# Kernel optimization log

Hardware: AMD Instinct MI355X
Metric: run time of the kernel (lower is better)

## Reference

```python
import jax, jax.numpy as jnp
import numpy as np

H = 64        # hidden_dim
A = 21        # N_ACTIONS
B = 262144    # batch size


def setup_inputs() -> dict:
    key = jax.random.key(0)
    ks = jax.random.split(key, 32)

    def w(k, shape):
        fan_in = shape[0]
        return (jax.random.normal(k, shape, jnp.float32) / np.float32(np.sqrt(fan_in)))

    inp = {
        "x": jax.random.normal(ks[0], (B, 2, 2), jnp.float32),
        "b_act1": jax.random.randint(ks[1], (B,), 0, A),
        "b_act2": jax.random.randint(ks[2], (B,), 0, A),
        # enc: Linear(2,H), ReLU, Linear(H,H), ReLU
        "enc_w1": w(ks[3], (2, H)), "enc_b1": jnp.zeros((H,), jnp.float32),
        "enc_w2": w(ks[4], (H, H)), "enc_b2": jnp.zeros((H,), jnp.float32),
        # q_net: Linear(H,H), ReLU, Linear(H,A)
        "q_w1": w(ks[5], (H, H)), "q_b1": jnp.zeros((H,), jnp.float32),
        "q_w2": w(ks[6], (H, A)), "q_b2": jnp.zeros((A,), jnp.float32),
        # v_net: Linear(H,H), ReLU, Linear(H,1)
        "v_w1": w(ks[7], (H, H)), "v_b1": jnp.zeros((H,), jnp.float32),
        "v_w2": w(ks[8], (H, 1)), "v_b2": jnp.zeros((1,), jnp.float32),
        # lin2: Linear(H+A,H), ReLU, Linear(H,H), ReLU, Linear(H,H)
        "l2_w1": w(ks[9], (H + A, H)), "l2_b1": jnp.zeros((H,), jnp.float32),
        "l2_w2": w(ks[10], (H, H)), "l2_b2": jnp.zeros((H,), jnp.float32),
        "l2_w3": w(ks[11], (H, H)), "l2_b3": jnp.zeros((H,), jnp.float32),
        # lin3, lin4
        "l3_w": w(ks[12], (H, H)), "l3_b": jnp.zeros((H,), jnp.float32),
        "l4_w": w(ks[13], (H, A)), "l4_b": jnp.zeros((A,), jnp.float32),
        # q_prime_net: Linear(H,2H) ELU Linear(2H,H) ELU Linear(H,H) ELU Linear(H,1)
        "qp_w1": w(ks[14], (H, 2 * H)), "qp_b1": jnp.zeros((2 * H,), jnp.float32),
        "qp_w2": w(ks[15], (2 * H, H)), "qp_b2": jnp.zeros((H,), jnp.float32),
        "qp_w3": w(ks[16], (H, H)), "qp_b3": jnp.zeros((H,), jnp.float32),
        "qp_w4": w(ks[17], (H, 1)), "qp_b4": jnp.zeros((1,), jnp.float32),
    }
    return inp


def reference(x, b_act1, b_act2,
              enc_w1, enc_b1, enc_w2, enc_b2,
              q_w1, q_b1, q_w2, q_b2,
              v_w1, v_b1, v_w2, v_b2,
              l2_w1, l2_b1, l2_w2, l2_b2, l2_w3, l2_b3,
              l3_w, l3_b, l4_w, l4_b,
              qp_w1, qp_b1, qp_w2, qp_b2, qp_w3, qp_b3, qp_w4, qp_b4):
    relu = jax.nn.relu
    elu = jax.nn.elu

    def enc(z):
        return relu(relu(z @ enc_w1 + enc_b1) @ enc_w2 + enc_b2)

    def q_net(h):
        return relu(h @ q_w1 + q_b1) @ q_w2 + q_b2

    def lin2(e):  # ends with bare Linear (no final activation)
        h = relu(e @ l2_w1 + l2_b1)
        h = relu(h @ l2_w2 + l2_b2)
        return h @ l2_w3 + l2_b3

    def q_prime(z):
        h = elu(z @ qp_w1 + qp_b1)
        h = elu(h @ qp_w2 + qp_b2)
        h = elu(h @ qp_w3 + qp_b3)
        return h @ qp_w4 + qp_b4

    h1 = enc(x[:, 0, :])  # [B,H]
    h2 = enc(x[:, 1, :])
    q1, q2 = q_net(h1), q_net(h2)              # [B,A]
    key2 = jnp.stack([h1, h2], axis=1)          # [B,2,H]
    vtot = relu((h1 + h2) @ v_w1 + v_b1) @ v_w2 + v_b2  # [B,1]

    def joint(act1, act2):
        oh1 = jax.nn.one_hot(act1, A, dtype=h1.dtype)
        oh2 = jax.nn.one_hot(act2, A, dtype=h2.dtype)
        e = jnp.stack([jnp.concatenate([h1, oh1], axis=-1),
                       jnp.concatenate([h2, oh2], axis=-1)], axis=1)  # [B,2,H+A]
        key1 = lin2(e)                              # [B,2,H]
        q = q_prime(key1.mean(axis=1))              # [B,1]
        return key1, q

    key1, joint_qs = joint(b_act1, b_act2)
    a1_max = jnp.argmax(q1, axis=1)
    a2_max = jnp.argmax(q2, axis=1)
    key1_max, joint_max_qs = joint(a1_max, a2_max)

    def q_jt(k1):
        z = key2 + k1.mean(axis=1, keepdims=True) - k1 / 2  # [B,2,H]
        return relu(z @ l3_w + l3_b) @ l4_w + l4_b           # [B,2,A]

    q_jt_alt = q_jt(key1)
    q_jt_max_alt = q_jt(key1_max)

    return (q1, q2, joint_qs, joint_max_qs, vtot, q_jt_alt, q_jt_max_alt)
```

## Files before the change

### kernel.cpp

```cpp
#include <hip/hip_runtime.h>
#include <hip/hip_bf16.h>


#define B_TOT 262144

typedef __bf16 bf16_t;
typedef __bf16 bf16x4 __attribute__((ext_vector_type(4)));
typedef __bf16 bf16x8 __attribute__((ext_vector_type(8)));
typedef float  f32x4  __attribute__((ext_vector_type(4)));

#define MFMA16(a, b, c) __builtin_amdgcn_mfma_f32_16x16x32_bf16((a), (b), (c), 0, 0, 0)

enum : int {
  OFF_VW1  = 0,
  OFF_L2W1 = 4096,
  OFF_L2W2 = 8192,
  OFF_L2W3 = 12288,
  OFF_L3W  = 16384,
  OFF_L4W  = 20480,
  OFF_QP1  = 22528,
  OFF_QP2  = 30720,
  OFF_QP3  = 38912,
  WS_ELEMS = 43008
};
#define WS_BYTES (WS_ELEMS * 2)

enum : int {
  O_Q1   = 0,
  O_Q2   = 21 * B_TOT,
  O_JQ   = 42 * B_TOT,
  O_JMQ  = 43 * B_TOT,
  O_VT   = 44 * B_TOT,
  O_QJT  = 45 * B_TOT,
  O_QJTM = 87 * B_TOT
};

struct RDesc { const float* src; int K; int N; int NT; int off; };
struct RPack { RDesc d[9]; };

__global__ void repack_kernel(RPack P, bf16_t* __restrict__ ws) {
  RDesc d = P.d[blockIdx.x];
  int n = (d.K >> 5) * d.NT * 512;
  for (int i = threadIdx.x; i < n; i += blockDim.x) {
    int j  = i & 7;
    int l  = (i >> 3) & 63;
    int t  = i >> 9;
    int nt = t % d.NT;
    int kc = t / d.NT;
    int sk = kc * 32 + 16 * (j >> 2) + 4 * (l >> 4) + (j & 3);
    int sn = nt * 16 + (l & 15);
    float v = (sn < d.N) ? d.src[sk * d.N + sn] : 0.0f;
    ws[d.off + i] = (bf16_t)v;
  }
}

struct Args {
  const float* x; const int* a1; const int* a2;
  const float* ew1; const float* eb1; const float* ew2; const float* eb2;
  const float* qw1; const float* qb1; const float* qw2; const float* qb2;
  const float* vw1; const float* vb1; const float* vw2; const float* vb2;
  const float* l2w1; const float* l2b1; const float* l2w2; const float* l2b2;
  const float* l2w3; const float* l2b3;
  const float* l3w;  const float* l3b;  const float* l4w;  const float* l4b;
  const float* qpw1; const float* qpb1; const float* qpw2; const float* qpb2;
  const float* qpw3; const float* qpb3; const float* qpw4; const float* qpb4;
  float* out; const bf16_t* ws;
};

struct __align__(16) SMem {
  bf16_t h1b[64 * 72];
  bf16_t h2b[64 * 72];
  unsigned char scr[34816];
  float  bias[768];
  bf16_t oneh[21 * 68];
  int    acts[128];
  int    amax[128];
  float  red[64][2];
  int    redi[64][2];
};

__device__ __forceinline__ float eluf(float x) { return x > 0.f ? x : expm1f(x); }

__device__ __forceinline__ void fcA64(const float* __restrict__ fin, float* __restrict__ fout,
                                      const float* __restrict__ W, const float* __restrict__ Bv,
                                      bf16_t* hb, int r, int g) {
  float2 acc[8];
#pragma unroll
  for (int i = 0; i < 8; i++) acc[i] = make_float2(Bv[g * 16 + 2 * i], Bv[g * 16 + 2 * i + 1]);
#pragma unroll 4
  for (int k4 = 0; k4 < 16; k4++) {
    float4 a = *(const float4*)(fin + r * 68 + k4 * 4);
    float av[4] = {a.x, a.y, a.z, a.w};
#pragma unroll
    for (int kk = 0; kk < 4; kk++) {
      const float2* wr = (const float2*)(W + (k4 * 4 + kk) * 64 + g * 16);
#pragma unroll
      for (int i = 0; i < 8; i++) {
        float2 w = wr[i];
        acc[i].x = fmaf(av[kk], w.x, acc[i].x);
        acc[i].y = fmaf(av[kk], w.y, acc[i].y);
      }
    }
  }
#pragma unroll
  for (int i = 0; i < 8; i++) {
    float v0 = fmaxf(acc[i].x, 0.f), v1 = fmaxf(acc[i].y, 0.f);
    fout[r * 68 + g * 16 + 2 * i]     = v0;
    fout[r * 68 + g * 16 + 2 * i + 1] = v1;
    if (hb) {
      hb[r * 72 + g * 16 + 2 * i]     = (bf16_t)v0;
      hb[r * 72 + g * 16 + 2 * i + 1] = (bf16_t)v1;
    }
  }
}

template <int NC>
__device__ __forceinline__ void qn2(const float* __restrict__ fin, const float* __restrict__ W21,
                                    const float* __restrict__ Bv, float* __restrict__ qo,
                                    int r, int colbase, float& bv, int& bi) {
  float acc[NC];
#pragma unroll
  for (int i = 0; i < NC; i++) acc[i] = Bv[colbase + i];
  for (int k4 = 0; k4 < 16; k4++) {
    float4 a = *(const float4*)(fin + r * 68 + k4 * 4);
    float av[4] = {a.x, a.y, a.z, a.w};
#pragma unroll
    for (int kk = 0; kk < 4; kk++) {
      const float* wr = W21 + (k4 * 4 + kk) * 21 + colbase;
#pragma unroll
      for (int i = 0; i < NC; i++) acc[i] = fmaf(av[kk], wr[i], acc[i]);
    }
  }
  bv = -3e38f; bi = 0;
#pragma unroll
  for (int i = 0; i < NC; i++) {
    qo[i] = acc[i];
    if (acc[i] > bv) { bv = acc[i]; bi = colbase + i; }
  }
}

template <bool USEWS, int NT, int KC>
__device__ __forceinline__ f32x4 tileT(const bf16x8* __restrict__ WF,
                                       const float* __restrict__ Wp, int N, int woff,
                                       const bf16x8* __restrict__ bin,
                                       const float* __restrict__ bias, int bbase,
                                       int nt, int l, int c, int u) {
  f32x4 a = *(const f32x4*)(bias + bbase + nt * 16 + 4 * u);
#pragma unroll
  for (int kc = 0; kc < KC; kc++) {
    bf16x8 w;
    if constexpr (USEWS) {
      w = WF[(woff >> 3) + (kc * NT + nt) * 64 + l];
    } else {
      int sn = nt * 16 + c;
      if (sn < N) {
#pragma unroll
        for (int j = 0; j < 8; j++)
          w[j] = (bf16_t)Wp[(kc * 32 + 16 * (j >> 2) + 4 * u + (j & 3)) * N + sn];
      } else {
#pragma unroll
        for (int j = 0; j < 8; j++) w[j] = (bf16_t)0.0f;
      }
    }
    a = MFMA16(w, bin[kc], a);
  }
  return a;
}

template <int MODE>
__device__ __forceinline__ bf16x8 pack2(f32x4 t0, f32x4 t1) {
  bf16x8 r;
#pragma unroll
  for (int j = 0; j < 8; j++) {
    float v = (j >> 2) ? t1[j & 3] : t0[j & 3];
    if constexpr (MODE == 1) v = fmaxf(v, 0.f);
    if constexpr (MODE == 2) v = eluf(v);
    r[j] = (bf16_t)v;
  }
  return r;
}

template <bool USEWS>
__global__ __launch_bounds__(256, 2) void qtran_main(Args A) {
  __shared__ SMem sm;
  const int t = threadIdx.x;
  const int wgbase = blockIdx.x * 64;
  const int r = t & 63;
  const int g = __builtin_amdgcn_readfirstlane(t >> 6);

  float* f0 = (float*)sm.scr;
  float* f1 = f0 + 64 * 68;

  if (t < 64) {
    sm.bias[t]        = A.vb1[t];
    sm.bias[64 + t]   = A.l2b1[t];
    sm.bias[128 + t]  = A.l2b2[t];
    sm.bias[192 + t]  = A.l2b3[t];
    sm.bias[384 + t]  = A.qpb2[t];
    sm.bias[448 + t]  = A.qpb3[t];
    sm.bias[512 + t]  = A.l3b[t];
    sm.bias[608 + t]  = A.vw2[t];
    sm.bias[672 + t]  = A.qpw4[t];
    sm.acts[t]        = A.a1[wgbase + t];
    sm.acts[64 + t]   = A.a2[wgbase + t];
  } else if (t < 192) {
    sm.bias[256 + t - 64] = A.qpb1[t - 64];
  } else if (t < 224) {
    int i = t - 192;
    sm.bias[576 + i] = (i < 21) ? A.l4b[i] : 0.0f;
  } else if (t == 224) {
    sm.bias[736] = A.vb2[0];
    sm.bias[737] = A.qpb4[0];
  }
  for (int i = t; i < 21 * 68; i += 256) {
    int a_ = i / 68, n_ = i % 68;
    sm.oneh[i] = (bf16_t)((n_ < 64) ? A.l2w1[(64 + a_) * 64 + n_] : 0.0f);
  }

  const int rowg = wgbase + r;
  float4 xv = ((const float4*)A.x)[rowg];
#pragma unroll 1
  for (int s = 0; s < 2; ++s) {
    float xa = s ? xv.z : xv.x;
    float xb = s ? xv.w : xv.y;
#pragma unroll
    for (int cc = 0; cc < 16; cc++) {
      int col = g * 16 + cc;
      float h = fmaf(xa, A.ew1[col], fmaf(xb, A.ew1[64 + col], A.eb1[col]));
      f0[r * 68 + col] = fmaxf(h, 0.f);
    }
    __syncthreads();
    fcA64(f0, f1, A.ew2, A.eb2, s ? sm.h2b : sm.h1b, r, g);
    __syncthreads();
    fcA64(f1, f0, A.qw1, A.qb1, nullptr, r, g);
    __syncthreads();
    {
      float* qo = A.out + (s ? O_Q2 : O_Q1) + rowg * 21;
      float bv; int bi;
      if (g == 0) {
        qn2<16>(f0, A.qw2, A.qb2, qo, r, 0, bv, bi);
        sm.red[r][0] = bv; sm.redi[r][0] = bi;
      } else if (g == 1) {
        qn2<5>(f0, A.qw2, A.qb2, qo + 16, r, 16, bv, bi);
        sm.red[r][1] = bv; sm.redi[r][1] = bi;
      }
    }
    __syncthreads();
    if (t < 64)
      sm.amax[s * 64 + t] = (sm.red[t][0] >= sm.red[t][1]) ? sm.redi[t][0] : sm.redi[t][1];
    __syncthreads();
  }
  __syncthreads();

  const int l = t & 63;
  const int c = l & 15, u = l >> 4;
  const int rb = g * 16;
  const int row = rb + c;
  float* out = A.out;
  const bf16x8* WF = (const bf16x8*)A.ws;
  const float* bias = sm.bias;
  float* S = (float*)sm.scr;

  auto HG = [&](const bf16_t* __restrict__ HB, int kc) -> bf16x8 {
    const bf16_t* p = HB + row * 72 + kc * 32 + 4 * u;
    bf16x4 lo = *(const bf16x4*)p;
    bf16x4 hi = *(const bf16x4*)(p + 16);
    bf16x8 rr;
#pragma unroll
    for (int d = 0; d < 4; d++) { rr[d] = lo[d]; rr[4 + d] = hi[d]; }
    return rr;
  };

  {
    bf16x8 aS[2];
#pragma unroll
    for (int kc = 0; kc < 2; kc++) {
      bf16x8 a1 = HG(sm.h1b, kc), a2 = HG(sm.h2b, kc);
      bf16x8 s8;
#pragma unroll
      for (int i = 0; i < 8; i++) s8[i] = (bf16_t)((float)a1[i] + (float)a2[i]);
      aS[kc] = s8;
    }
    float pr = 0.f;
#pragma unroll
    for (int nt = 0; nt < 4; nt++) {
      f32x4 tv = tileT<USEWS, 4, 2>(WF, A.vw1, 64, OFF_VW1, aS, bias, 0, nt, l, c, u);
      f32x4 wv = *(const f32x4*)(bias + 608 + nt * 16 + 4 * u);
#pragma unroll
      for (int p = 0; p < 4; p++) pr += fmaxf(tv[p], 0.f) * wv[p];
    }
    pr += __shfl_xor(pr, 16, 64);
    pr += __shfl_xor(pr, 32, 64);
    if (u == 0) out[O_VT + wgbase + row] = pr + bias[736];
  }

  auto J = [&](const int* __restrict__ av1, const int* __restrict__ av2,
               int jointBase, int qjtBase) {
    bf16x8 k1f[2][2];
    f32x4 msum[4];
#pragma unroll
    for (int j = 0; j < 2; j++) {
      const bf16_t* HB = j ? sm.h2b : sm.h1b;
      const int act = (j ? av2 : av1)[row];
      bf16x8 bh[2];
#pragma unroll
      for (int kc = 0; kc < 2; kc++) bh[kc] = HG(HB, kc);
      bf16x8 b1[2];
#pragma unroll
      for (int f = 0; f < 2; f++) {
        f32x4 t0 = tileT<USEWS, 4, 2>(WF, A.l2w1, 64, OFF_L2W1, bh, bias, 64, 2 * f, l, c, u);
        f32x4 t1 = tileT<USEWS, 4, 2>(WF, A.l2w1, 64, OFF_L2W1, bh, bias, 64, 2 * f + 1, l, c, u);
        bf16x4 oh0 = *(const bf16x4*)(sm.oneh + act * 68 + (2 * f) * 16 + 4 * u);
        bf16x4 oh1 = *(const bf16x4*)(sm.oneh + act * 68 + (2 * f + 1) * 16 + 4 * u);
#pragma unroll
        for (int p = 0; p < 4; p++) { t0[p] += (float)oh0[p]; t1[p] += (float)oh1[p]; }
        b1[f] = pack2<1>(t0, t1);
      }
      bf16x8 b2[2];
#pragma unroll
      for (int f = 0; f < 2; f++) {
        f32x4 t0 = tileT<USEWS, 4, 2>(WF, A.l2w2, 64, OFF_L2W2, b1, bias, 128, 2 * f, l, c, u);
        f32x4 t1 = tileT<USEWS, 4, 2>(WF, A.l2w2, 64, OFF_L2W2, b1, bias, 128, 2 * f + 1, l, c, u);
        b2[f] = pack2<1>(t0, t1);
      }
#pragma unroll
      for (int f = 0; f < 2; f++) {
        f32x4 t0 = tileT<USEWS, 4, 2>(WF, A.l2w3, 64, OFF_L2W3, b2, bias, 192, 2 * f, l, c, u);
        f32x4 t1 = tileT<USEWS, 4, 2>(WF, A.l2w3, 64, OFF_L2W3, b2, bias, 192, 2 * f + 1, l, c, u);
        k1f[j][f] = pack2<0>(t0, t1);
        if (j == 0) { msum[2 * f] = t0; msum[2 * f + 1] = t1; }
        else        { msum[2 * f] += t0; msum[2 * f + 1] += t1; }
      }
    }
    bf16x8 aM[2];
#pragma unroll
    for (int kc = 0; kc < 2; kc++) {
      f32x4 m0 = 0.5f * msum[2 * kc], m1 = 0.5f * msum[2 * kc + 1];
      aM[kc] = pack2<0>(m0, m1);
    }
    bf16x8 bq[4];
#pragma unroll
    for (int f = 0; f < 4; f++) {
      f32x4 t0 = tileT<USEWS, 8, 2>(WF, A.qpw1, 128, OFF_QP1, aM, bias, 256, 2 * f, l, c, u);
      f32x4 t1 = tileT<USEWS, 8, 2>(WF, A.qpw1, 128, OFF_QP1, aM, bias, 256, 2 * f + 1, l, c, u);
      bq[f] = pack2<2>(t0, t1);
    }
    bf16x8 b3[2];
#pragma unroll
    for (int f = 0; f < 2; f++) {
      f32x4 t0 = tileT<USEWS, 4, 4>(WF, A.qpw2, 64, OFF_QP2, bq, bias, 384, 2 * f, l, c, u);
      f32x4 t1 = tileT<USEWS, 4, 4>(WF, A.qpw2, 64, OFF_QP2, bq, bias, 384, 2 * f + 1, l, c, u);
      b3[f] = pack2<2>(t0, t1);
    }
    {
      float pj = 0.f;
#pragma unroll
      for (int nt = 0; nt < 4; nt++) {
        f32x4 tq = tileT<USEWS, 4, 2>(WF, A.qpw3, 64, OFF_QP3, b3, bias, 448, nt, l, c, u);
        f32x4 w4 = *(const f32x4*)(bias + 672 + nt * 16 + 4 * u);
#pragma unroll
        for (int p = 0; p < 4; p++) pj += eluf(tq[p]) * w4[p];
      }
      pj += __shfl_xor(pj, 16, 64);
      pj += __shfl_xor(pj, 32, 64);
      if (u == 0) out[jointBase + wgbase + row] = pj + bias[737];
    }
#pragma unroll
    for (int j = 0; j < 2; j++) {
      const bf16_t* HB = j ? sm.h2b : sm.h1b;
      bf16x8 aZ[2];
#pragma unroll
      for (int kc = 0; kc < 2; kc++) {
        bf16x8 h8 = HG(HB, kc);
        bf16x8 kk = k1f[1 - j][kc];
#pragma unroll
        for (int i = 0; i < 8; i++)
          aZ[kc][i] = (bf16_t)((float)h8[i] + 0.5f * (float)kk[i]);
      }
      bf16x8 bz[2];
#pragma unroll
      for (int f = 0; f < 2; f++) {
        f32x4 t0 = tileT<USEWS, 4, 2>(WF, A.l3w, 64, OFF_L3W, aZ, bias, 512, 2 * f, l, c, u);
        f32x4 t1 = tileT<USEWS, 4, 2>(WF, A.l3w, 64, OFF_L3W, aZ, bias, 512, 2 * f + 1, l, c, u);
        bz[f] = pack2<1>(t0, t1);
      }
#pragma unroll
      for (int nt = 0; nt < 2; nt++) {
        f32x4 tq = tileT<USEWS, 2, 2>(WF, A.l4w, 21, OFF_L4W, bz, bias, 576, nt, l, c, u);
#pragma unroll
        for (int p = 0; p < 4; p++) {
          int n2 = nt * 16 + 4 * u + p;
          if (n2 < 21) S[row * 43 + j * 21 + n2] = tq[p];
        }
      }
    }
    __syncthreads();
    const int ob = qjtBase + wgbase * 42;
    for (int i = t; i < 64 * 42; i += 256) out[ob + i] = S[(i / 42) * 43 + (i % 42)];
    __syncthreads();
  };

  J(sm.acts, sm.acts + 64, O_JQ, O_QJT);
  J(sm.amax, sm.amax + 64, O_JMQ, O_QJTM);
}

extern "C" void kernel_launch(void* const* d_in, const int* in_sizes, int n_in,
                              void* d_out, int out_size, void* d_ws, size_t ws_size,
                              hipStream_t stream) {
  (void)in_sizes; (void)n_in; (void)out_size;
  Args A;
  A.x    = (const float*)d_in[0];
  A.a1   = (const int*)d_in[1];
  A.a2   = (const int*)d_in[2];
  A.ew1  = (const float*)d_in[3];
  A.eb1  = (const float*)d_in[4];
  A.ew2  = (const float*)d_in[5];
  A.eb2  = (const float*)d_in[6];
  A.qw1  = (const float*)d_in[7];
  A.qb1  = (const float*)d_in[8];
  A.qw2  = (const float*)d_in[9];
  A.qb2  = (const float*)d_in[10];
  A.vw1  = (const float*)d_in[11];
  A.vb1  = (const float*)d_in[12];
  A.vw2  = (const float*)d_in[13];
  A.vb2  = (const float*)d_in[14];
  A.l2w1 = (const float*)d_in[15];
  A.l2b1 = (const float*)d_in[16];
  A.l2w2 = (const float*)d_in[17];
  A.l2b2 = (const float*)d_in[18];
  A.l2w3 = (const float*)d_in[19];
  A.l2b3 = (const float*)d_in[20];
  A.l3w  = (const float*)d_in[21];
  A.l3b  = (const float*)d_in[22];
  A.l4w  = (const float*)d_in[23];
  A.l4b  = (const float*)d_in[24];
  A.qpw1 = (const float*)d_in[25];
  A.qpb1 = (const float*)d_in[26];
  A.qpw2 = (const float*)d_in[27];
  A.qpb2 = (const float*)d_in[28];
  A.qpw3 = (const float*)d_in[29];
  A.qpb3 = (const float*)d_in[30];
  A.qpw4 = (const float*)d_in[31];
  A.qpb4 = (const float*)d_in[32];
  A.out  = (float*)d_out;
  A.ws   = (const bf16_t*)d_ws;

  if (ws_size >= (size_t)WS_BYTES) {
    bf16_t* ws = (bf16_t*)d_ws;
    RPack P;
    P.d[0] = {A.vw1,  64, 64,  4, OFF_VW1};
    P.d[1] = {A.l2w1, 64, 64,  4, OFF_L2W1};
    P.d[2] = {A.l2w2, 64, 64,  4, OFF_L2W2};
    P.d[3] = {A.l2w3, 64, 64,  4, OFF_L2W3};
    P.d[4] = {A.l3w,  64, 64,  4, OFF_L3W};
    P.d[5] = {A.l4w,  64, 21,  2, OFF_L4W};
    P.d[6] = {A.qpw1, 64, 128, 8, OFF_QP1};
    P.d[7] = {A.qpw2, 128, 64, 4, OFF_QP2};
    P.d[8] = {A.qpw3, 64, 64,  4, OFF_QP3};
    hipLaunchKernelGGL(repack_kernel, dim3(9), dim3(256), 0, stream, P, ws);
    hipLaunchKernelGGL(HIP_KERNEL_NAME(qtran_main<true>), dim3(B_TOT / 64), dim3(256), 0,
                       stream, A);
  } else {
    hipLaunchKernelGGL(HIP_KERNEL_NAME(qtran_main<false>), dim3(B_TOT / 64), dim3(256), 0,
                       stream, A);
  }
}
```

Measured before the change: 945.7 us.

## Share lin2 first-layer matmul across both action sets and interleave joint passes

```diff
diff --git a/kernel.cpp b/kernel.cpp
--- a/kernel.cpp
+++ b/kernel.cpp
@@ -7,6 +7,7 @@
 typedef __bf16 bf16_t;
 typedef __bf16 bf16x4 __attribute__((ext_vector_type(4)));
 typedef __bf16 bf16x8 __attribute__((ext_vector_type(8)));
+typedef float  f32x2  __attribute__((ext_vector_type(2)));
 typedef float  f32x4  __attribute__((ext_vector_type(4)));
 
 #define MFMA16(a, b, c) __builtin_amdgcn_mfma_f32_16x16x32_bf16((a), (b), (c), 0, 0, 0)
@@ -84,29 +85,27 @@
 __device__ __forceinline__ void fcA64(const float* __restrict__ fin, float* __restrict__ fout,
                                       const float* __restrict__ W, const float* __restrict__ Bv,
                                       bf16_t* hb, int r, int g) {
-  float2 acc[8];
-#pragma unroll
-  for (int i = 0; i < 8; i++) acc[i] = make_float2(Bv[g * 16 + 2 * i], Bv[g * 16 + 2 * i + 1]);
+  f32x2 acc[8];
+  const f32x2* Bv2 = (const f32x2*)(Bv + g * 16);
+#pragma unroll
+  for (int i = 0; i < 8; i++) acc[i] = Bv2[i];
 #pragma unroll 4
   for (int k4 = 0; k4 < 16; k4++) {
     float4 a = *(const float4*)(fin + r * 68 + k4 * 4);
     float av[4] = {a.x, a.y, a.z, a.w};
 #pragma unroll
     for (int kk = 0; kk < 4; kk++) {
-      const float2* wr = (const float2*)(W + (k4 * 4 + kk) * 64 + g * 16);
-#pragma unroll
-      for (int i = 0; i < 8; i++) {
-        float2 w = wr[i];
-        acc[i].x = fmaf(av[kk], w.x, acc[i].x);
-        acc[i].y = fmaf(av[kk], w.y, acc[i].y);
-      }
+      const f32x2* wr = (const f32x2*)(W + (k4 * 4 + kk) * 64 + g * 16);
+      f32x2 avv = {av[kk], av[kk]};
+#pragma unroll
+      for (int i = 0; i < 8; i++) acc[i] += avv * wr[i];
     }
   }
 #pragma unroll
   for (int i = 0; i < 8; i++) {
-    float v0 = fmaxf(acc[i].x, 0.f), v1 = fmaxf(acc[i].y, 0.f);
-    fout[r * 68 + g * 16 + 2 * i]     = v0;
-    fout[r * 68 + g * 16 + 2 * i + 1] = v1;
+    float v0 = fmaxf(acc[i][0], 0.f), v1 = fmaxf(acc[i][1], 0.f);
+    f32x2 v = {v0, v1};
+    *(f32x2*)(fout + r * 68 + g * 16 + 2 * i) = v;
     if (hb) {
       hb[r * 72 + g * 16 + 2 * i]     = (bf16_t)v0;
       hb[r * 72 + g * 16 + 2 * i + 1] = (bf16_t)v1;
@@ -294,88 +293,73 @@
     if (u == 0) out[O_VT + wgbase + row] = pr + bias[736];
   }
 
-  auto J = [&](const int* __restrict__ av1, const int* __restrict__ av2,
-               int jointBase, int qjtBase) {
-    bf16x8 k1f[2][2];
-    f32x4 msum[4];
-#pragma unroll
-    for (int j = 0; j < 2; j++) {
-      const bf16_t* HB = j ? sm.h2b : sm.h1b;
-      const int act = (j ? av2 : av1)[row];
-      bf16x8 bh[2];
-#pragma unroll
-      for (int kc = 0; kc < 2; kc++) bh[kc] = HG(HB, kc);
-      bf16x8 b1[2];
+  const int* actsrc[2] = {sm.acts, sm.amax};
+  bf16x8 k1f[2][2][2];
+  f32x4 msum[2][4];
+
+#pragma unroll
+  for (int j = 0; j < 2; j++) {
+    const bf16_t* HB = j ? sm.h2b : sm.h1b;
+    bf16x8 bh[2];
+#pragma unroll
+    for (int kc = 0; kc < 2; kc++) bh[kc] = HG(HB, kc);
+    f32x4 tS[4];
+#pragma unroll
+    for (int nt = 0; nt < 4; nt++)
+      tS[nt] = tileT<USEWS, 4, 2>(WF, A.l2w1, 64, OFF_L2W1, bh, bias, 64, nt, l, c, u);
+    bf16x8 b1[2][2];
+#pragma unroll
+    for (int x = 0; x < 2; x++) {
+      const int act = actsrc[x][j * 64 + row];
+      f32x4 tt0 = tS[0], tt1 = tS[1], tt2 = tS[2], tt3 = tS[3];
+      bf16x4 oh0 = *(const bf16x4*)(sm.oneh + act * 68 + 0 * 16 + 4 * u);
+      bf16x4 oh1 = *(const bf16x4*)(sm.oneh + act * 68 + 1 * 16 + 4 * u);
+      bf16x4 oh2 = *(const bf16x4*)(sm.oneh + act * 68 + 2 * 16 + 4 * u);
+      bf16x4 oh3 = *(const bf16x4*)(sm.oneh + act * 68 + 3 * 16 + 4 * u);
+#pragma unroll
+      for (int p = 0; p < 4; p++) {
+        tt0[p] += (float)oh0[p]; tt1[p] += (float)oh1[p];
+        tt2[p] += (float)oh2[p]; tt3[p] += (float)oh3[p];
+      }
+      b1[x][0] = pack2<1>(tt0, tt1);
+      b1[x][1] = pack2<1>(tt2, tt3);
+    }
+    bf16x8 b2[2][2];
+#pragma unroll
+    for (int x = 0; x < 2; x++)
 #pragma unroll
       for (int f = 0; f < 2; f++) {
-        f32x4 t0 = tileT<USEWS, 4, 2>(WF, A.l2w1, 64, OFF_L2W1, bh, bias, 64, 2 * f, l, c, u);
-        f32x4 t1 = tileT<USEWS, 4, 2>(WF, A.l2w1, 64, OFF_L2W1, bh, bias, 64, 2 * f + 1, l, c, u);
-        bf16x4 oh0 = *(const bf16x4*)(sm.oneh + act * 68 + (2 * f) * 16 + 4 * u);
-        bf16x4 oh1 = *(const bf16x4*)(sm.oneh + act * 68 + (2 * f + 1) * 16 + 4 * u);
-#pragma unroll
-        for (int p = 0; p < 4; p++) { t0[p] += (float)oh0[p]; t1[p] += (float)oh1[p]; }
-        b1[f] = pack2<1>(t0, t1);
-      }
-      bf16x8 b2[2];
+        f32x4 t0 = tileT<USEWS, 4, 2>(WF, A.l2w2, 64, OFF_L2W2, b1[x], bias, 128, 2 * f, l, c, u);
+        f32x4 t1 = tileT<USEWS, 4, 2>(WF, A.l2w2, 64, OFF_L2W2, b1[x], bias, 128, 2 * f + 1, l, c, u);
+        b2[x][f] = pack2<1>(t0, t1);
+      }
+#pragma unroll
+    for (int x = 0; x < 2; x++)
 #pragma unroll
       for (int f = 0; f < 2; f++) {
-        f32x4 t0 = tileT<USEWS, 4, 2>(WF, A.l2w2, 64, OFF_L2W2, b1, bias, 128, 2 * f, l, c, u);
-        f32x4 t1 = tileT<USEWS, 4, 2>(WF, A.l2w2, 64, OFF_L2W2, b1, bias, 128, 2 * f + 1, l, c, u);
-        b2[f] = pack2<1>(t0, t1);
-      }
-#pragma unroll
-      for (int f = 0; f < 2; f++) {
-        f32x4 t0 = tileT<USEWS, 4, 2>(WF, A.l2w3, 64, OFF_L2W3, b2, bias, 192, 2 * f, l, c, u);
-        f32x4 t1 = tileT<USEWS, 4, 2>(WF, A.l2w3, 64, OFF_L2W3, b2, bias, 192, 2 * f + 1, l, c, u);
-        k1f[j][f] = pack2<0>(t0, t1);
-        if (j == 0) { msum[2 * f] = t0; msum[2 * f + 1] = t1; }
-        else        { msum[2 * f] += t0; msum[2 * f + 1] += t1; }
-      }
-    }
-    bf16x8 aM[2];
-#pragma unroll
-    for (int kc = 0; kc < 2; kc++) {
-      f32x4 m0 = 0.5f * msum[2 * kc], m1 = 0.5f * msum[2 * kc + 1];
-      aM[kc] = pack2<0>(m0, m1);
-    }
-    bf16x8 bq[4];
-#pragma unroll
-    for (int f = 0; f < 4; f++) {
-      f32x4 t0 = tileT<USEWS, 8, 2>(WF, A.qpw1, 128, OFF_QP1, aM, bias, 256, 2 * f, l, c, u);
-      f32x4 t1 = tileT<USEWS, 8, 2>(WF, A.qpw1, 128, OFF_QP1, aM, bias, 256, 2 * f + 1, l, c, u);
-      bq[f] = pack2<2>(t0, t1);
-    }
-    bf16x8 b3[2];
-#pragma unroll
-    for (int f = 0; f < 2; f++) {
-      f32x4 t0 = tileT<USEWS, 4, 4>(WF, A.qpw2, 64, OFF_QP2, bq, bias, 384, 2 * f, l, c, u);
-      f32x4 t1 = tileT<USEWS, 4, 4>(WF, A.qpw2, 64, OFF_QP2, bq, bias, 384, 2 * f + 1, l, c, u);
-      b3[f] = pack2<2>(t0, t1);
-    }
-    {
-      float pj = 0.f;
-#pragma unroll
-      for (int nt = 0; nt < 4; nt++) {
-        f32x4 tq = tileT<USEWS, 4, 2>(WF, A.qpw3, 64, OFF_QP3, b3, bias, 448, nt, l, c, u);
-        f32x4 w4 = *(const f32x4*)(bias + 672 + nt * 16 + 4 * u);
-#pragma unroll
-        for (int p = 0; p < 4; p++) pj += eluf(tq[p]) * w4[p];
-      }
-      pj += __shfl_xor(pj, 16, 64);
-      pj += __shfl_xor(pj, 32, 64);
-      if (u == 0) out[jointBase + wgbase + row] = pj + bias[737];
-    }
-#pragma unroll
-    for (int j = 0; j < 2; j++) {
-      const bf16_t* HB = j ? sm.h2b : sm.h1b;
+        f32x4 t0 = tileT<USEWS, 4, 2>(WF, A.l2w3, 64, OFF_L2W3, b2[x], bias, 192, 2 * f, l, c, u);
+        f32x4 t1 = tileT<USEWS, 4, 2>(WF, A.l2w3, 64, OFF_L2W3, b2[x], bias, 192, 2 * f + 1, l, c, u);
+        k1f[x][j][f] = pack2<0>(t0, t1);
+        if (j == 0) { msum[x][2 * f] = t0; msum[x][2 * f + 1] = t1; }
+        else        { msum[x][2 * f] += t0; msum[x][2 * f + 1] += t1; }
+      }
+  }
+
+#pragma unroll
+  for (int j = 0; j < 2; j++) {
+    const bf16_t* HB = j ? sm.h2b : sm.h1b;
+    bf16x8 h8[2];
+#pragma unroll
+    for (int kc = 0; kc < 2; kc++) h8[kc] = HG(HB, kc);
+#pragma unroll
+    for (int x = 0; x < 2; x++) {
       bf16x8 aZ[2];
 #pragma unroll
       for (int kc = 0; kc < 2; kc++) {
-        bf16x8 h8 = HG(HB, kc);
-        bf16x8 kk = k1f[1 - j][kc];
+        bf16x8 kk = k1f[x][1 - j][kc];
 #pragma unroll
         for (int i = 0; i < 8; i++)
-          aZ[kc][i] = (bf16_t)((float)h8[i] + 0.5f * (float)kk[i]);
+          aZ[kc][i] = (bf16_t)((float)h8[kc][i] + 0.5f * (float)kk[i]);
       }
       bf16x8 bz[2];
 #pragma unroll
@@ -390,18 +374,65 @@
 #pragma unroll
         for (int p = 0; p < 4; p++) {
           int n2 = nt * 16 + 4 * u + p;
-          if (n2 < 21) S[row * 43 + j * 21 + n2] = tq[p];
+          if (n2 < 21) S[x * 2752 + row * 43 + j * 21 + n2] = tq[p];
         }
       }
     }
-    __syncthreads();
-    const int ob = qjtBase + wgbase * 42;
-    for (int i = t; i < 64 * 42; i += 256) out[ob + i] = S[(i / 42) * 43 + (i % 42)];
-    __syncthreads();
-  };
-
-  J(sm.acts, sm.acts + 64, O_JQ, O_QJT);
-  J(sm.amax, sm.amax + 64, O_JMQ, O_QJTM);
+  }
+
+  {
+    bf16x8 aM[2][2];
+#pragma unroll
+    for (int x = 0; x < 2; x++)
+#pragma unroll
+      for (int kc = 0; kc < 2; kc++) {
+        f32x4 m0 = 0.5f * msum[x][2 * kc], m1 = 0.5f * msum[x][2 * kc + 1];
+        aM[x][kc] = pack2<0>(m0, m1);
+      }
+    bf16x8 bq[2][4];
+#pragma unroll
+    for (int x = 0; x < 2; x++)
+#pragma unroll
+      for (int f = 0; f < 4; f++) {
+        f32x4 t0 = tileT<USEWS, 8, 2>(WF, A.qpw1, 128, OFF_QP1, aM[x], bias, 256, 2 * f, l, c, u);
+        f32x4 t1 = tileT<USEWS, 8, 2>(WF, A.qpw1, 128, OFF_QP1, aM[x], bias, 256, 2 * f + 1, l, c, u);
+        bq[x][f] = pack2<2>(t0, t1);
+      }
+    bf16x8 b3[2][2];
+#pragma unroll
+    for (int x = 0; x < 2; x++)
+#pragma unroll
+      for (int f = 0; f < 2; f++) {
+        f32x4 t0 = tileT<USEWS, 4, 4>(WF, A.qpw2, 64, OFF_QP2, bq[x], bias, 384, 2 * f, l, c, u);
+        f32x4 t1 = tileT<USEWS, 4, 4>(WF, A.qpw2, 64, OFF_QP2, bq[x], bias, 384, 2 * f + 1, l, c, u);
+        b3[x][f] = pack2<2>(t0, t1);
+      }
+    float pj[2] = {0.f, 0.f};
+#pragma unroll
+    for (int x = 0; x < 2; x++)
+#pragma unroll
+      for (int nt = 0; nt < 4; nt++) {
+        f32x4 tq = tileT<USEWS, 4, 2>(WF, A.qpw3, 64, OFF_QP3, b3[x], bias, 448, nt, l, c, u);
+        f32x4 w4 = *(const f32x4*)(bias + 672 + nt * 16 + 4 * u);
+#pragma unroll
+        for (int p = 0; p < 4; p++) pj[x] += eluf(tq[p]) * w4[p];
+      }
+#pragma unroll
+    for (int x = 0; x < 2; x++) {
+      float v = pj[x];
+      v += __shfl_xor(v, 16, 64);
+      v += __shfl_xor(v, 32, 64);
+      if (u == 0) out[(x ? O_JMQ : O_JQ) + wgbase + row] = v + bias[737];
+    }
+  }
+
+#pragma unroll
+  for (int x = 0; x < 2; x++) {
+    const int ob = (x ? O_QJTM : O_QJT) + (wgbase + rb) * 42;
+    const float* Sx = S + x * 2752 + rb * 43;
+    for (int i2 = l; i2 < 672; i2 += 64)
+      out[ob + i2] = Sx[(i2 / 42) * 43 + (i2 % 42)];
+  }
 }
 
 extern "C" void kernel_launch(void* const* d_in, const int* in_sizes, int n_in,
```

New measurement: 908.0 us. 1.04x faster.
